# Optimization experiments

Measured on AMD Instinct MI355X. Metric: run time of the kernel, lower is better.

## Reference

```python
import jax, jax.numpy as jnp
import numpy as np

D_MODEL = 1024
NUM_HEADS = 16
D_K = D_MODEL // NUM_HEADS
B, S = 2, 2048


def setup_inputs() -> dict:
    key = jax.random.key(0)
    ks = jax.random.split(key, 4)
    scale = 1.0 / np.sqrt(D_MODEL)
    x = jax.random.normal(ks[0], (B, S, D_MODEL), dtype=jnp.float32)
    w_qkv = jax.random.normal(ks[1], (D_MODEL, 3 * D_MODEL), dtype=jnp.float32) * scale
    b_qkv = jnp.zeros((3 * D_MODEL,), dtype=jnp.float32)
    w_out = jax.random.normal(ks[2], (D_MODEL, D_MODEL), dtype=jnp.float32) * scale
    b_out = jnp.zeros((D_MODEL,), dtype=jnp.float32)
    # causal mask: 1 where attention is allowed (j <= i), 0 elsewhere
    mask = jnp.tril(jnp.ones((S, S), dtype=jnp.int32))
    return {"x": x, "mask": mask, "w_qkv": w_qkv, "b_qkv": b_qkv,
            "w_out": w_out, "b_out": b_out}


def reference(x, mask, w_qkv, b_qkv, w_out, b_out):
    Bb, Ss, C = x.shape
    qkv = x @ w_qkv + b_qkv                      # [B,S,3C]
    q, k, v = jnp.split(qkv, 3, axis=-1)
    def split_heads(t):
        return t.reshape(Bb, Ss, NUM_HEADS, D_K).transpose(0, 2, 1, 3)  # [B,H,S,Dk]
    q, k, v = split_heads(q), split_heads(k), split_heads(v)
    scores = jnp.einsum('bhqd,bhkd->bhqk', q, k) / jnp.sqrt(jnp.float32(D_K))
    scores = jnp.where(mask == 0, -jnp.inf, scores)
    weights = jax.nn.softmax(scores, axis=-1)
    weights = jnp.nan_to_num(weights, nan=0.0)   # matches torch.nan_to_num
    attn = jnp.einsum('bhqk,bhkd->bhqd', weights, v)
    attn = attn.transpose(0, 2, 1, 3).reshape(Bb, Ss, C)
    return attn @ w_out + b_out
```

## Files before the change

kernel.cpp:

```cpp
#include <hip/hip_runtime.h>
#include <hip/hip_bf16.h>

#define D_MODEL 1024
#define NUM_HEADS 16
#define D_K 64
#define BATCH 2
#define SEQ 2048

typedef __attribute__((ext_vector_type(8))) short bf16x8;
typedef __attribute__((ext_vector_type(4))) float f32x4;

union P16 { int4 i4; ushort u[8]; };
union FU { float f; unsigned int u; };

__device__ __forceinline__ float bf2f(ushort u) {
    union { unsigned int i; float f; } c; c.i = ((unsigned int)u) << 16; return c.f;
}
__device__ __forceinline__ ushort f2bf(float f) {
    union { float f; unsigned int i; } c; c.f = f;
    unsigned int x = c.i;
    return (ushort)((x + 0x7fff + ((x >> 16) & 1)) >> 16);
}

__device__ __forceinline__ bool wave_detect_f32(const ushort* x) {
    ushort u = x[2 * (threadIdx.x & 63)];
    int e = (u >> 7) & 0xFF;
    unsigned long long bl = __ballot(e >= 100 && e <= 141);
    return __popcll(bl) < 32;
}

__global__ __launch_bounds__(256)
void prep_all(const ushort* __restrict__ x, const void* __restrict__ Wq,
              const void* __restrict__ Wo, ushort* __restrict__ xb,
              ushort* __restrict__ WqT, ushort* __restrict__ WoT,
              int* __restrict__ flag)
{
    const bool f32 = wave_detect_f32(x);
    const int bx = blockIdx.x, tx = threadIdx.x;
    if (bx == 0 && tx == 0) flag[0] = f32 ? 1 : 0;

    if (bx >= 1024) {
        if (!f32) return;
        int i = ((bx - 1024) * 256 + tx) * 8;
        const float* f = (const float*)x + i;
        float4 a = *(const float4*)f, b = *(const float4*)(f + 4);
        P16 r;
        r.u[0] = f2bf(a.x); r.u[1] = f2bf(a.y); r.u[2] = f2bf(a.z); r.u[3] = f2bf(a.w);
        r.u[4] = f2bf(b.x); r.u[5] = f2bf(b.y); r.u[6] = f2bf(b.z); r.u[7] = f2bf(b.w);
        *(int4*)(xb + i) = r.i4;
        return;
    }

    __shared__ ushort t[64][72];
    const int nb = bx & 63, kb = bx >> 6;
    const void* W; ushort* WT; int N, n0;
    if (nb < 48) { W = Wq; WT = WqT; N = 3 * D_MODEL; n0 = nb * 64; }
    else         { W = Wo; WT = WoT; N = D_MODEL;     n0 = (nb - 48) * 64; }
    const int k0 = kb * 64, K = D_MODEL;
    #pragma unroll
    for (int p = 0; p < 16; ++p) {
        int r = p * 4 + (tx >> 6), c = tx & 63;
        float v = f32 ? ((const float*)W)[(size_t)(k0 + r) * N + n0 + c]
                      : bf2f(((const ushort*)W)[(size_t)(k0 + r) * N + n0 + c]);
        t[r][c] = f2bf(v);
    }
    __syncthreads();
    #pragma unroll
    for (int p = 0; p < 16; ++p) {
        int nn = p * 4 + (tx >> 6), kk = tx & 63;
        WT[(size_t)(n0 + nn) * K + k0 + kk] = t[kk][nn];
    }
}

template<int MODE>
__global__ __launch_bounds__(256)
void gemm128(const void* __restrict__ Araw, const ushort* __restrict__ Aconv,
             const ushort* __restrict__ WT, const void* __restrict__ bias,
             void* __restrict__ out, int N, int K, const int* __restrict__ flag)
{
    __shared__ ushort As[2][128 * 32];
    __shared__ ushort Bs[2][128 * 32];

    const int f = *flag;
    const ushort* A = (MODE == 1) ? (f ? Aconv : (const ushort*)Araw) : Aconv;

    const int tid = threadIdx.x;
    const int w = tid >> 6, lane = tid & 63;
    const int ln = lane & 15, quad = lane >> 4;
    const int m0 = blockIdx.y * 128, n0 = blockIdx.x * 128;
    const int wm = (w >> 1) * 64, wn = (w & 1) * 64;

    const int s0 = w * 128 + lane, s1 = s0 + 64;
    const int ar0 = s0 >> 2, ak0 = ((s0 & 3) ^ ((ar0 >> 1) & 3)) * 8;
    const int ar1 = s1 >> 2, ak1 = ((s1 & 3) ^ ((ar1 >> 1) & 3)) * 8;
    const size_t aoff0 = (size_t)(m0 + ar0) * K + ak0;
    const size_t aoff1 = (size_t)(m0 + ar1) * K + ak1;
    const size_t boff0 = (size_t)(n0 + ar0) * K + ak0;
    const size_t boff1 = (size_t)(n0 + ar1) * K + ak1;

    const int physc = (quad ^ ((ln >> 1) & 3)) * 8;

    f32x4 acc[4][4] = {};

    const int nk = K >> 5;
    int4 a0 = *(const int4*)(A + aoff0);
    int4 a1 = *(const int4*)(A + aoff1);
    int4 b0 = *(const int4*)(WT + boff0);
    int4 b1 = *(const int4*)(WT + boff1);
    *(int4*)(As[0] + s0 * 8) = a0;
    *(int4*)(As[0] + s1 * 8) = a1;
    *(int4*)(Bs[0] + s0 * 8) = b0;
    *(int4*)(Bs[0] + s1 * 8) = b1;
    a0 = *(const int4*)(A + aoff0 + 32);
    a1 = *(const int4*)(A + aoff1 + 32);
    b0 = *(const int4*)(WT + boff0 + 32);
    b1 = *(const int4*)(WT + boff1 + 32);
    __syncthreads();

    for (int kt = 0; kt < nk; ++kt) {
        const int cur = kt & 1;
        if (kt + 1 < nk) {
            *(int4*)(As[1 - cur] + s0 * 8) = a0;
            *(int4*)(As[1 - cur] + s1 * 8) = a1;
            *(int4*)(Bs[1 - cur] + s0 * 8) = b0;
            *(int4*)(Bs[1 - cur] + s1 * 8) = b1;
        }
        if (kt + 2 < nk) {
            const int kc = (kt + 2) * 32;
            a0 = *(const int4*)(A + aoff0 + kc);
            a1 = *(const int4*)(A + aoff1 + kc);
            b0 = *(const int4*)(WT + boff0 + kc);
            b1 = *(const int4*)(WT + boff1 + kc);
        }

        bf16x8 af[4], bf[4];
        #pragma unroll
        for (int t = 0; t < 4; ++t) {
            af[t] = *(const bf16x8*)(As[cur] + (wm + t * 16 + ln) * 32 + physc);
            bf[t] = *(const bf16x8*)(Bs[cur] + (wn + t * 16 + ln) * 32 + physc);
        }
        #pragma unroll
        for (int mi = 0; mi < 4; ++mi)
            #pragma unroll
            for (int ni = 0; ni < 4; ++ni)
                acc[mi][ni] = __builtin_amdgcn_mfma_f32_16x16x32_bf16(
                    af[mi], bf[ni], acc[mi][ni], 0, 0, 0);
        __syncthreads();
    }

    #pragma unroll
    for (int mi = 0; mi < 4; ++mi) {
        #pragma unroll
        for (int ni = 0; ni < 4; ++ni) {
            int col = n0 + wn + ni * 16 + ln;
            float bb = f ? ((const float*)bias)[col] : bf2f(((const ushort*)bias)[col]);
            #pragma unroll
            for (int r = 0; r < 4; ++r) {
                int row = m0 + wm + mi * 16 + quad * 4 + r;
                float v = acc[mi][ni][r] + bb;
                if (MODE == 0 && f) ((float*)out)[(size_t)row * N + col] = v;
                else                ((ushort*)out)[(size_t)row * N + col] = f2bf(v);
            }
        }
    }
}

__global__ __launch_bounds__(256)
void flash_attn8(const ushort* __restrict__ qkv, ushort* __restrict__ attn)
{
    __shared__ ushort Ks[2][64][72];
    __shared__ ushort Vs[2][64][72];
    __shared__ ushort QPs[128][72];

    const int tid  = threadIdx.x;
    const int wave = tid >> 6, lane = tid & 63;
    const int ln   = lane & 15, quad = lane >> 4;
    const int pg   = wave >> 1, ww = wave & 1;
    const int bh   = blockIdx.x;
    const int ky   = blockIdx.y;
    const int k    = (ky < 8) ? ky : 23 - ky;
    const int xx   = 2 * k + pg;
    const int b    = bh >> 4, hh = bh & (NUM_HEADS - 1);
    const int W3   = 3 * D_MODEL;
    const size_t hbase = (size_t)b * SEQ * W3 + hh * D_K;

    const int q0A = 32 * (63 - xx), q0B = 32 * xx;
    const int ntA = 32 - k, ntB = k + 1;

    const int qrr = tid >> 1, qcol = (tid & 1) * 32;
    const int ksr = tid >> 2, ksc = (tid & 3) * 16;
    const int vp  = tid & 31, vg = (tid >> 5) * 8;

    {
        const int qpg = qrr >> 6, qmt = (qrr >> 5) & 1, ql = qrr & 31;
        const int qxx = 2 * k + qpg;
        const int grow = qmt ? (32 * qxx + ql) : (32 * (63 - qxx) + ql);
        const ushort* src = qkv + hbase + (size_t)grow * W3 + qcol;
        #pragma unroll
        for (int h = 0; h < 4; ++h) {
            P16 v; v.i4 = *(const int4*)(src + h * 8);
            #pragma unroll
            for (int e = 0; e < 8; ++e) v.u[e] = f2bf(bf2f(v.u[e]) * 0.18033688011f);
            *(int4*)(&QPs[qrr][qcol + h * 8]) = v.i4;
        }
    }

    const ushort* Kbase = qkv + hbase + D_MODEL;
    const ushort* Vbase = qkv + hbase + 2 * D_MODEL;

    int4 kreg[2], vreg[2];
    {
        const ushort* ksrc = Kbase + (size_t)ksr * W3 + ksc;
        kreg[0] = *(const int4*)(ksrc);
        kreg[1] = *(const int4*)(ksrc + 8);
        vreg[0] = *(const int4*)(Vbase + (size_t)(2 * vp)     * W3 + vg);
        vreg[1] = *(const int4*)(Vbase + (size_t)(2 * vp + 1) * W3 + vg);
    }
    *(int4*)(&Ks[0][ksr][ksc])     = kreg[0];
    *(int4*)(&Ks[0][ksr][ksc + 8]) = kreg[1];
    {
        P16 v0, v1; v0.i4 = vreg[0]; v1.i4 = vreg[1];
        #pragma unroll
        for (int e = 0; e < 8; ++e) {
            unsigned int pack = (unsigned int)v0.u[e] | ((unsigned int)v1.u[e] << 16);
            *(unsigned int*)(&Vs[0][vg + e][2 * vp]) = pack;
        }
    }
    {
        const ushort* ksrc = Kbase + (size_t)(64 + ksr) * W3 + ksc;
        kreg[0] = *(const int4*)(ksrc);
        kreg[1] = *(const int4*)(ksrc + 8);
        vreg[0] = *(const int4*)(Vbase + (size_t)(64 + 2 * vp)     * W3 + vg);
        vreg[1] = *(const int4*)(Vbase + (size_t)(64 + 2 * vp + 1) * W3 + vg);
    }
    __syncthreads();

    bf16x8 qf[2][2];
    #pragma unroll
    for (int mt = 0; mt < 2; ++mt)
        #pragma unroll
        for (int s = 0; s < 2; ++s)
            qf[mt][s] = *(const bf16x8*)(&QPs[pg * 64 + mt * 32 + ww * 16 + ln][s * 32 + quad * 8]);

    f32x4 acc_o[2][4] = {};
    f32x4 acc_l[2] = {};

    bf16x8 ones8;
    #pragma unroll
    for (int e = 0; e < 8; ++e) ones8[e] = (short)0x3F80;

    for (int jt = 0; jt < ntA; ++jt) {
        const int cur = jt & 1;
        const int j0 = jt * 64;
        const bool doB = (jt < ntB);

        if (jt + 1 < ntA) {
            *(int4*)(&Ks[1 - cur][ksr][ksc])     = kreg[0];
            *(int4*)(&Ks[1 - cur][ksr][ksc + 8]) = kreg[1];
            P16 v0, v1; v0.i4 = vreg[0]; v1.i4 = vreg[1];
            #pragma unroll
            for (int e = 0; e < 8; ++e) {
                unsigned int pack = (unsigned int)v0.u[e] | ((unsigned int)v1.u[e] << 16);
                *(unsigned int*)(&Vs[1 - cur][vg + e][2 * vp]) = pack;
            }
        }
        if (jt + 2 < ntA) {
            const int jn = j0 + 128;
            const ushort* ksrc = Kbase + (size_t)(jn + ksr) * W3 + ksc;
            kreg[0] = *(const int4*)(ksrc);
            kreg[1] = *(const int4*)(ksrc + 8);
            vreg[0] = *(const int4*)(Vbase + (size_t)(jn + 2 * vp)     * W3 + vg);
            vreg[1] = *(const int4*)(Vbase + (size_t)(jn + 2 * vp + 1) * W3 + vg);
        }

        f32x4 sa[2][4];
        #pragma unroll
        for (int t = 0; t < 4; ++t) {
            bf16x8 k0 = *(const bf16x8*)(&Ks[cur][t * 16 + ln][quad * 8]);
            bf16x8 k1 = *(const bf16x8*)(&Ks[cur][t * 16 + ln][32 + quad * 8]);
            {
                f32x4 z = {};
                z = __builtin_amdgcn_mfma_f32_16x16x32_bf16(qf[0][0], k0, z, 0, 0, 0);
                z = __builtin_amdgcn_mfma_f32_16x16x32_bf16(qf[0][1], k1, z, 0, 0, 0);
                sa[0][t] = z;
            }
            if (doB) {
                f32x4 z = {};
                z = __builtin_amdgcn_mfma_f32_16x16x32_bf16(qf[1][0], k0, z, 0, 0, 0);
                z = __builtin_amdgcn_mfma_f32_16x16x32_bf16(qf[1][1], k1, z, 0, 0, 0);
                sa[1][t] = z;
            }
        }

        if (jt == ntA - 1) {
            const int rowb = q0A + ww * 16 + quad * 4;
            #pragma unroll
            for (int t = 0; t < 4; ++t)
                #pragma unroll
                for (int r = 0; r < 4; ++r)
                    if (j0 + t * 16 + ln > rowb + r) sa[0][t][r] = -1e30f;
        }
        if (doB && jt == ntB - 1) {
            const int rowb = q0B + ww * 16 + quad * 4;
            #pragma unroll
            for (int t = 0; t < 4; ++t)
                #pragma unroll
                for (int r = 0; r < 4; ++r)
                    if (j0 + t * 16 + ln > rowb + r) sa[1][t][r] = -1e30f;
        }

        const int lnx = ln ^ ((quad & 1) * 8);
        #pragma unroll
        for (int mt = 0; mt < 2; ++mt) {
            if (mt && !doB) break;
            #pragma unroll
            for (int r = 0; r < 4; ++r) {
                const int prow = pg * 64 + mt * 32 + ww * 16 + quad * 4 + r;
                #pragma unroll
                for (int t = 0; t < 4; ++t) {
                    FU cc; cc.f = exp2f(sa[mt][t][r]);
                    QPs[prow][((t ^ (quad >> 1)) * 16) + lnx] = (ushort)(cc.u >> 16);
                }
            }
        }

        #pragma unroll
        for (int s = 0; s < 2; ++s) {
            const int pcol = s * 32 + ((quad ^ ((ln >> 2) & 3)) * 8);
            bf16x8 pf0 = *(const bf16x8*)(&QPs[pg * 64 + ww * 16 + ln][pcol]);
            bf16x8 pf1;
            if (doB) pf1 = *(const bf16x8*)(&QPs[pg * 64 + 32 + ww * 16 + ln][pcol]);
            #pragma unroll
            for (int t = 0; t < 4; ++t) {
                bf16x8 vf = *(const bf16x8*)(&Vs[cur][t * 16 + ln][s * 32 + quad * 8]);
                acc_o[0][t] = __builtin_amdgcn_mfma_f32_16x16x32_bf16(pf0, vf, acc_o[0][t], 0, 0, 0);
                if (doB)
                    acc_o[1][t] = __builtin_amdgcn_mfma_f32_16x16x32_bf16(pf1, vf, acc_o[1][t], 0, 0, 0);
            }
            acc_l[0] = __builtin_amdgcn_mfma_f32_16x16x32_bf16(pf0, ones8, acc_l[0], 0, 0, 0);
            if (doB)
                acc_l[1] = __builtin_amdgcn_mfma_f32_16x16x32_bf16(pf1, ones8, acc_l[1], 0, 0, 0);
        }

        __syncthreads();
    }

    #pragma unroll
    for (int mt = 0; mt < 2; ++mt) {
        const int q0 = mt ? q0B : q0A;
        #pragma unroll
        for (int r = 0; r < 4; ++r) {
            float inv = 1.0f / acc_l[mt][r];
            int i = q0 + ww * 16 + quad * 4 + r;
            size_t rowoff = ((size_t)(b * SEQ + i)) * D_MODEL + hh * D_K;
            #pragma unroll
            for (int t = 0; t < 4; ++t)
                attn[rowoff + t * 16 + ln] = f2bf(acc_o[mt][t][r] * inv);
        }
    }
}

extern "C" void kernel_launch(void* const* d_in, const int* in_sizes, int n_in,
                              void* d_out, int out_size, void* d_ws, size_t ws_size,
                              hipStream_t stream)
{
    const void* x     = d_in[0];
    const void* w_qkv = d_in[2];
    const void* b_qkv = d_in[3];
    const void* w_out = d_in[4];
    const void* b_out = d_in[5];

    char* ws = (char*)d_ws;
    int*    flag   = (int*)ws;                  size_t off = 256;
    ushort* WqkvT  = (ushort*)(ws + off);       off += (size_t)3 * D_MODEL * D_MODEL * 2;
    ushort* WoutT  = (ushort*)(ws + off);       off += (size_t)D_MODEL * D_MODEL * 2;
    ushort* qkv_ws = (ushort*)(ws + off);       off += (size_t)BATCH * SEQ * 3 * D_MODEL * 2;
    ushort* xb     = (ushort*)(ws + off);
    ushort* attn_ws = xb;

    const int M = BATCH * SEQ;

    prep_all<<<3072, 256, 0, stream>>>((const ushort*)x, w_qkv, w_out,
                                       xb, WqkvT, WoutT, flag);

    gemm128<1><<<dim3(3 * D_MODEL / 128, M / 128), 256, 0, stream>>>(
        x, xb, WqkvT, b_qkv, qkv_ws, 3 * D_MODEL, D_MODEL, flag);

    dim3 ga(BATCH * NUM_HEADS, 16);
    flash_attn8<<<ga, 256, 0, stream>>>(qkv_ws, attn_ws);

    gemm128<0><<<dim3(D_MODEL / 128, M / 128), 256, 0, stream>>>(
        attn_ws, attn_ws, WoutT, b_out, d_out, D_MODEL, D_MODEL, flag);
}
```

Measured before the change: 232.1 us.

## Process two KV tiles per barrier pair with two-tile register prefetch

Restructures the flash-attention KV loop so each iteration stores two prefetched K/V tiles into both LDS buffers at once. It then issues global loads for the next two tiles and computes both tiles back to back. The aim is to amortise barrier and loop overhead over twice the work and to give the global loads more latency slack. In exchange, the LDS stores no longer overlap with compute on the other buffer, and the prefetch registers double, which raises VGPR pressure.

```diff
diff --git a/kernel.cpp b/kernel.cpp
--- a/kernel.cpp
+++ b/kernel.cpp
@@ -166,7 +166,7 @@
 }
 
 __global__ __launch_bounds__(256)
-void flash_attn8(const ushort* __restrict__ qkv, ushort* __restrict__ attn)
+void flash_attn9(const ushort* __restrict__ qkv, ushort* __restrict__ attn)
 {
     __shared__ ushort Ks[2][64][72];
     __shared__ ushort Vs[2][64][72];
@@ -208,30 +208,15 @@
     const ushort* Kbase = qkv + hbase + D_MODEL;
     const ushort* Vbase = qkv + hbase + 2 * D_MODEL;
 
-    int4 kreg[2], vreg[2];
-    {
-        const ushort* ksrc = Kbase + (size_t)ksr * W3 + ksc;
-        kreg[0] = *(const int4*)(ksrc);
-        kreg[1] = *(const int4*)(ksrc + 8);
-        vreg[0] = *(const int4*)(Vbase + (size_t)(2 * vp)     * W3 + vg);
-        vreg[1] = *(const int4*)(Vbase + (size_t)(2 * vp + 1) * W3 + vg);
-    }
-    *(int4*)(&Ks[0][ksr][ksc])     = kreg[0];
-    *(int4*)(&Ks[0][ksr][ksc + 8]) = kreg[1];
-    {
-        P16 v0, v1; v0.i4 = vreg[0]; v1.i4 = vreg[1];
-        #pragma unroll
-        for (int e = 0; e < 8; ++e) {
-            unsigned int pack = (unsigned int)v0.u[e] | ((unsigned int)v1.u[e] << 16);
-            *(unsigned int*)(&Vs[0][vg + e][2 * vp]) = pack;
-        }
-    }
-    {
-        const ushort* ksrc = Kbase + (size_t)(64 + ksr) * W3 + ksc;
-        kreg[0] = *(const int4*)(ksrc);
-        kreg[1] = *(const int4*)(ksrc + 8);
-        vreg[0] = *(const int4*)(Vbase + (size_t)(64 + 2 * vp)     * W3 + vg);
-        vreg[1] = *(const int4*)(Vbase + (size_t)(64 + 2 * vp + 1) * W3 + vg);
+    int4 kreg[2][2], vreg[2][2];
+    #pragma unroll
+    for (int u = 0; u < 2; ++u) {
+        const int jr = u * 64;
+        const ushort* ksrc = Kbase + (size_t)(jr + ksr) * W3 + ksc;
+        kreg[u][0] = *(const int4*)(ksrc);
+        kreg[u][1] = *(const int4*)(ksrc + 8);
+        vreg[u][0] = *(const int4*)(Vbase + (size_t)(jr + 2 * vp)     * W3 + vg);
+        vreg[u][1] = *(const int4*)(Vbase + (size_t)(jr + 2 * vp + 1) * W3 + vg);
     }
     __syncthreads();
 
@@ -249,100 +234,111 @@
     #pragma unroll
     for (int e = 0; e < 8; ++e) ones8[e] = (short)0x3F80;
 
-    for (int jt = 0; jt < ntA; ++jt) {
-        const int cur = jt & 1;
-        const int j0 = jt * 64;
-        const bool doB = (jt < ntB);
-
-        if (jt + 1 < ntA) {
-            *(int4*)(&Ks[1 - cur][ksr][ksc])     = kreg[0];
-            *(int4*)(&Ks[1 - cur][ksr][ksc + 8]) = kreg[1];
-            P16 v0, v1; v0.i4 = vreg[0]; v1.i4 = vreg[1];
+    for (int jt2 = 0; jt2 < ntA; jt2 += 2) {
+        __syncthreads();
+
+        #pragma unroll
+        for (int u = 0; u < 2; ++u) {
+            if (u && jt2 + 1 >= ntA) break;
+            *(int4*)(&Ks[u][ksr][ksc])     = kreg[u][0];
+            *(int4*)(&Ks[u][ksr][ksc + 8]) = kreg[u][1];
+            P16 v0, v1; v0.i4 = vreg[u][0]; v1.i4 = vreg[u][1];
             #pragma unroll
             for (int e = 0; e < 8; ++e) {
                 unsigned int pack = (unsigned int)v0.u[e] | ((unsigned int)v1.u[e] << 16);
-                *(unsigned int*)(&Vs[1 - cur][vg + e][2 * vp]) = pack;
-            }
-        }
-        if (jt + 2 < ntA) {
-            const int jn = j0 + 128;
-            const ushort* ksrc = Kbase + (size_t)(jn + ksr) * W3 + ksc;
-            kreg[0] = *(const int4*)(ksrc);
-            kreg[1] = *(const int4*)(ksrc + 8);
-            vreg[0] = *(const int4*)(Vbase + (size_t)(jn + 2 * vp)     * W3 + vg);
-            vreg[1] = *(const int4*)(Vbase + (size_t)(jn + 2 * vp + 1) * W3 + vg);
-        }
-
-        f32x4 sa[2][4];
-        #pragma unroll
-        for (int t = 0; t < 4; ++t) {
-            bf16x8 k0 = *(const bf16x8*)(&Ks[cur][t * 16 + ln][quad * 8]);
-            bf16x8 k1 = *(const bf16x8*)(&Ks[cur][t * 16 + ln][32 + quad * 8]);
-            {
-                f32x4 z = {};
-                z = __builtin_amdgcn_mfma_f32_16x16x32_bf16(qf[0][0], k0, z, 0, 0, 0);
-                z = __builtin_amdgcn_mfma_f32_16x16x32_bf16(qf[0][1], k1, z, 0, 0, 0);
-                sa[0][t] = z;
-            }
-            if (doB) {
-                f32x4 z = {};
-                z = __builtin_amdgcn_mfma_f32_16x16x32_bf16(qf[1][0], k0, z, 0, 0, 0);
-                z = __builtin_amdgcn_mfma_f32_16x16x32_bf16(qf[1][1], k1, z, 0, 0, 0);
-                sa[1][t] = z;
-            }
-        }
-
-        if (jt == ntA - 1) {
-            const int rowb = q0A + ww * 16 + quad * 4;
-            #pragma unroll
-            for (int t = 0; t < 4; ++t)
+                *(unsigned int*)(&Vs[u][vg + e][2 * vp]) = pack;
+            }
+        }
+        __syncthreads();
+
+        #pragma unroll
+        for (int u = 0; u < 2; ++u) {
+            if (jt2 + 2 + u < ntA) {
+                const int jr = (jt2 + 2 + u) * 64;
+                const ushort* ksrc = Kbase + (size_t)(jr + ksr) * W3 + ksc;
+                kreg[u][0] = *(const int4*)(ksrc);
+                kreg[u][1] = *(const int4*)(ksrc + 8);
+                vreg[u][0] = *(const int4*)(Vbase + (size_t)(jr + 2 * vp)     * W3 + vg);
+                vreg[u][1] = *(const int4*)(Vbase + (size_t)(jr + 2 * vp + 1) * W3 + vg);
+            }
+        }
+
+        #pragma unroll
+        for (int u = 0; u < 2; ++u) {
+            const int jt = jt2 + u;
+            if (u && jt >= ntA) break;
+            const int j0 = jt * 64;
+            const bool doB = (jt < ntB);
+
+            f32x4 sa[2][4];
+            #pragma unroll
+            for (int t = 0; t < 4; ++t) {
+                bf16x8 k0 = *(const bf16x8*)(&Ks[u][t * 16 + ln][quad * 8]);
+                bf16x8 k1 = *(const bf16x8*)(&Ks[u][t * 16 + ln][32 + quad * 8]);
+                {
+                    f32x4 z = {};
+                    z = __builtin_amdgcn_mfma_f32_16x16x32_bf16(qf[0][0], k0, z, 0, 0, 0);
+                    z = __builtin_amdgcn_mfma_f32_16x16x32_bf16(qf[0][1], k1, z, 0, 0, 0);
+                    sa[0][t] = z;
+                }
+                if (doB) {
+                    f32x4 z = {};
+                    z = __builtin_amdgcn_mfma_f32_16x16x32_bf16(qf[1][0], k0, z, 0, 0, 0);
+                    z = __builtin_amdgcn_mfma_f32_16x16x32_bf16(qf[1][1], k1, z, 0, 0, 0);
+                    sa[1][t] = z;
+                }
+            }
+
+            if (jt == ntA - 1) {
+                const int rowb = q0A + ww * 16 + quad * 4;
                 #pragma unroll
-                for (int r = 0; r < 4; ++r)
-                    if (j0 + t * 16 + ln > rowb + r) sa[0][t][r] = -1e30f;
-        }
-        if (doB && jt == ntB - 1) {
-            const int rowb = q0B + ww * 16 + quad * 4;
-            #pragma unroll
-            for (int t = 0; t < 4; ++t)
+                for (int t = 0; t < 4; ++t)
+                    #pragma unroll
+                    for (int r = 0; r < 4; ++r)
+                        if (j0 + t * 16 + ln > rowb + r) sa[0][t][r] = -1e30f;
+            }
+            if (doB && jt == ntB - 1) {
+                const int rowb = q0B + ww * 16 + quad * 4;
                 #pragma unroll
-                for (int r = 0; r < 4; ++r)
-                    if (j0 + t * 16 + ln > rowb + r) sa[1][t][r] = -1e30f;
-        }
-
-        const int lnx = ln ^ ((quad & 1) * 8);
-        #pragma unroll
-        for (int mt = 0; mt < 2; ++mt) {
-            if (mt && !doB) break;
-            #pragma unroll
-            for (int r = 0; r < 4; ++r) {
-                const int prow = pg * 64 + mt * 32 + ww * 16 + quad * 4 + r;
+                for (int t = 0; t < 4; ++t)
+                    #pragma unroll
+                    for (int r = 0; r < 4; ++r)
+                        if (j0 + t * 16 + ln > rowb + r) sa[1][t][r] = -1e30f;
+            }
+
+            const int lnx = ln ^ ((quad & 1) * 8);
+            #pragma unroll
+            for (int mt = 0; mt < 2; ++mt) {
+                if (mt && !doB) break;
+                #pragma unroll
+                for (int r = 0; r < 4; ++r) {
+                    const int prow = pg * 64 + mt * 32 + ww * 16 + quad * 4 + r;
+                    #pragma unroll
+                    for (int t = 0; t < 4; ++t) {
+                        FU cc; cc.f = exp2f(sa[mt][t][r]);
+                        QPs[prow][((t ^ (quad >> 1)) * 16) + lnx] = (ushort)(cc.u >> 16);
+                    }
+                }
+            }
+
+            #pragma unroll
+            for (int s = 0; s < 2; ++s) {
+                const int pcol = s * 32 + ((quad ^ ((ln >> 2) & 3)) * 8);
+                bf16x8 pf0 = *(const bf16x8*)(&QPs[pg * 64 + ww * 16 + ln][pcol]);
+                bf16x8 pf1;
+                if (doB) pf1 = *(const bf16x8*)(&QPs[pg * 64 + 32 + ww * 16 + ln][pcol]);
                 #pragma unroll
                 for (int t = 0; t < 4; ++t) {
-                    FU cc; cc.f = exp2f(sa[mt][t][r]);
-                    QPs[prow][((t ^ (quad >> 1)) * 16) + lnx] = (ushort)(cc.u >> 16);
+                    bf16x8 vf = *(const bf16x8*)(&Vs[u][t * 16 + ln][s * 32 + quad * 8]);
+                    acc_o[0][t] = __builtin_amdgcn_mfma_f32_16x16x32_bf16(pf0, vf, acc_o[0][t], 0, 0, 0);
+                    if (doB)
+                        acc_o[1][t] = __builtin_amdgcn_mfma_f32_16x16x32_bf16(pf1, vf, acc_o[1][t], 0, 0, 0);
                 }
-            }
-        }
-
-        #pragma unroll
-        for (int s = 0; s < 2; ++s) {
-            const int pcol = s * 32 + ((quad ^ ((ln >> 2) & 3)) * 8);
-            bf16x8 pf0 = *(const bf16x8*)(&QPs[pg * 64 + ww * 16 + ln][pcol]);
-            bf16x8 pf1;
-            if (doB) pf1 = *(const bf16x8*)(&QPs[pg * 64 + 32 + ww * 16 + ln][pcol]);
-            #pragma unroll
-            for (int t = 0; t < 4; ++t) {
-                bf16x8 vf = *(const bf16x8*)(&Vs[cur][t * 16 + ln][s * 32 + quad * 8]);
-                acc_o[0][t] = __builtin_amdgcn_mfma_f32_16x16x32_bf16(pf0, vf, acc_o[0][t], 0, 0, 0);
+                acc_l[0] = __builtin_amdgcn_mfma_f32_16x16x32_bf16(pf0, ones8, acc_l[0], 0, 0, 0);
                 if (doB)
-                    acc_o[1][t] = __builtin_amdgcn_mfma_f32_16x16x32_bf16(pf1, vf, acc_o[1][t], 0, 0, 0);
-            }
-            acc_l[0] = __builtin_amdgcn_mfma_f32_16x16x32_bf16(pf0, ones8, acc_l[0], 0, 0, 0);
-            if (doB)
-                acc_l[1] = __builtin_amdgcn_mfma_f32_16x16x32_bf16(pf1, ones8, acc_l[1], 0, 0, 0);
-        }
-
-        __syncthreads();
+                    acc_l[1] = __builtin_amdgcn_mfma_f32_16x16x32_bf16(pf1, ones8, acc_l[1], 0, 0, 0);
+            }
+        }
     }
 
     #pragma unroll
@@ -387,7 +383,7 @@
         x, xb, WqkvT, b_qkv, qkv_ws, 3 * D_MODEL, D_MODEL, flag);
 
     dim3 ga(BATCH * NUM_HEADS, 16);
-    flash_attn8<<<ga, 256, 0, stream>>>(qkv_ws, attn_ws);
+    flash_attn9<<<ga, 256, 0, stream>>>(qkv_ws, attn_ws);
 
     gemm128<0><<<dim3(D_MODEL / 128, M / 128), 256, 0, stream>>>(
         attn_ws, attn_ws, WoutT, b_out, d_out, D_MODEL, D_MODEL, flag);
```

Result: no change. 232.6 us (+0.2%).
